# Kernel optimization log

Hardware: AMD Instinct MI355X
Metric: run time of the kernel (lower is better)

Reference implementation:

```python
import jax, jax.numpy as jnp
import numpy as np


def setup_inputs() -> dict:
    key = jax.random.key(0)
    k1, k2, k3, k4 = jax.random.split(key, 4)
    B, S, E, H = 8, 2048, 1024, 64
    x = jax.random.normal(k1, (B, S, E), dtype=jnp.float32)
    # nn.Linear(E, H, bias=False) weight is (H, E); we store transposed (E, H)
    scale = 1.0 / np.sqrt(E)
    Wk = jax.random.normal(k2, (E, H), dtype=jnp.float32) * scale
    Wq = jax.random.normal(k3, (E, H), dtype=jnp.float32) * scale
    Wv = jax.random.normal(k4, (E, H), dtype=jnp.float32) * scale
    return {"x": x, "Wk": Wk, "Wq": Wq, "Wv": Wv}


def reference(x, Wk, Wq, Wv):
    # x: (B, S, E); projections: (B, S, H)
    k = x @ Wk
    q = x @ Wq
    v = x @ Wv
    H = k.shape[-1]
    # scores: (B, S, S) with 1/sqrt(H) scaling as in the torch code
    scores = jnp.einsum("bqh,bkh->bqk", q, k) * (H ** -0.5)
    S = x.shape[1]
    causal = jnp.triu(jnp.full((S, S), -jnp.inf, dtype=scores.dtype), k=1)
    wei = jax.nn.softmax(scores + causal, axis=-1)
    # dropout p=0.0 -> identity
    return jnp.einsum("bqk,bkh->bqh", wei, v)
```

## Files before the change

kernel.cpp:

```cpp
#include <hip/hip_runtime.h>
#include <hip/hip_bf16.h>

typedef unsigned short ushort_t;
typedef __attribute__((ext_vector_type(8))) short short8;
typedef __attribute__((ext_vector_type(4))) short short4v;
typedef __attribute__((ext_vector_type(4))) float f32x4;

__device__ __forceinline__ float bf2f(ushort_t u) {
    unsigned int x = ((unsigned int)u) << 16;
    float f; __builtin_memcpy(&f, &x, 4); return f;
}
__device__ __forceinline__ ushort_t f2bf(float f) {
    __hip_bfloat16 h = __float2bfloat16(f);
    ushort_t u; __builtin_memcpy(&u, &h, 2); return u;
}
__device__ __forceinline__ unsigned packbf2(float a, float b) {
    return (unsigned)f2bf(a) | ((unsigned)f2bf(b) << 16);
}

__device__ __forceinline__ void gload16(const void* g, void* l) {
    __builtin_amdgcn_global_load_lds(
        (const __attribute__((address_space(1))) unsigned int*)g,
        (__attribute__((address_space(3))) unsigned int*)l, 16, 0, 0);
}

constexpr int E  = 1024;
constexpr int Hd = 64;
constexpr int S  = 2048;
constexpr int ROWS = 8 * 2048;
constexpr int NTOT = 192;
constexpr int LSTA = 88;
constexpr int BM   = 64;

__global__ __launch_bounds__(256)
void prep_wt(const float* __restrict__ Wk, const float* __restrict__ Wq,
             const float* __restrict__ Wv, ushort_t* __restrict__ WT)
{
    int idx = blockIdx.x * 256 + threadIdx.x;
    int n = idx >> 10;
    int kk = idx & 1023;
    const float* W = (n < 64) ? Wq : ((n < 128) ? Wk : Wv);
    int h = n & 63;
    WT[idx] = f2bf(W[kk * Hd + h]);
}

__global__ __launch_bounds__(512, 4)
void proj_v13(const float* __restrict__ x, const ushort_t* __restrict__ WT,
              ushort_t* __restrict__ qo, ushort_t* __restrict__ ko,
              ushort_t* __restrict__ vTo)
{
    __shared__ alignas(16) float    XS[2][BM * 64];
    __shared__ alignas(16) ushort_t WS[2][192 * 64];

    const int t    = threadIdx.x;
    const int w    = t >> 6;
    const int lane = t & 63;
    const int m    = lane & 15;
    const int g    = lane >> 4;
    const int rl   = m & 7;
    const int cg   = w & 3;
    const int mh   = w >> 2;
    const int rb   = blockIdx.x * BM;

    f32x4 accq[2], acck[2], accv[2];
    #pragma unroll
    for (int j = 0; j < 2; ++j) {
        accq[j] = (f32x4){0.f, 0.f, 0.f, 0.f};
        acck[j] = (f32x4){0.f, 0.f, 0.f, 0.f};
        accv[j] = (f32x4){0.f, 0.f, 0.f, 0.f};
    }

    const int xr0 = t >> 4,         xu0 = (t & 15) ^ (xr0 & 7);
    const int xr1 = (t + 512) >> 4, xu1 = (t & 15) ^ (xr1 & 7);
    const float* xsrc0 = x + (size_t)(rb + xr0) * E + xu0 * 4;
    const float* xsrc1 = x + (size_t)(rb + xr1) * E + xu1 * 4;

    const ushort_t* wsrc[3];
    #pragma unroll
    for (int j = 0; j < 3; ++j) {
        const int L  = j * 512 + t;
        const int wr = L >> 3;
        const int wu = (L & 7) ^ (wr & 7);
        wsrc[j] = WT + (size_t)wr * E + wu * 8;
    }

    int xiA[2][2], xiB[2][2];
    #pragma unroll
    for (int h = 0; h < 2; ++h)
        #pragma unroll
        for (int kt = 0; kt < 2; ++kt) {
            const int row = mh * 32 + h * 16 + m;
            const int U   = kt * 8 + 2 * g;
            xiA[h][kt] = (row * 16 + (U ^ rl)) * 4;
            xiB[h][kt] = (row * 16 + ((U + 1) ^ rl)) * 4;
        }
    int wiq[2], wik[2], wiv[2];
    #pragma unroll
    for (int kt = 0; kt < 2; ++kt) {
        const int U = kt * 4 + g;
        wiq[kt] = ((      cg * 16 + m) * 8 + (U ^ rl)) * 8;
        wik[kt] = ((64  + cg * 16 + m) * 8 + (U ^ rl)) * 8;
        wiv[kt] = ((128 + cg * 16 + m) * 8 + (U ^ rl)) * 8;
    }

    auto STAGE = [&](int buf, int c) {
        const int k0 = c * 64;
        char* xb = (char*)&XS[buf][0];
        char* wb = (char*)&WS[buf][0];
        gload16(xsrc0 + k0, xb + (size_t)t * 16);
        gload16(xsrc1 + k0, xb + (size_t)(t + 512) * 16);
        #pragma unroll
        for (int j = 0; j < 3; ++j)
            gload16(wsrc[j] + k0, wb + (size_t)(j * 512 + t) * 16);
    };

    auto COMPUTE = [&](int buf) {
        #pragma unroll
        for (int kt = 0; kt < 2; ++kt) {
            short8 fq = *(const short8*)&WS[buf][wiq[kt]];
            short8 fk = *(const short8*)&WS[buf][wik[kt]];
            short8 fv = *(const short8*)&WS[buf][wiv[kt]];
            #pragma unroll
            for (int h = 0; h < 2; ++h) {
                float4 A = *(const float4*)&XS[buf][xiA[h][kt]];
                float4 B = *(const float4*)&XS[buf][xiB[h][kt]];
                short8 a;
                {
                    unsigned u4[4];
                    u4[0] = packbf2(A.x, A.y);
                    u4[1] = packbf2(A.z, A.w);
                    u4[2] = packbf2(B.x, B.y);
                    u4[3] = packbf2(B.z, B.w);
                    __builtin_memcpy(&a, u4, 16);
                }
                accq[h] = __builtin_amdgcn_mfma_f32_16x16x32_bf16(a, fq, accq[h], 0, 0, 0);
                acck[h] = __builtin_amdgcn_mfma_f32_16x16x32_bf16(a, fk, acck[h], 0, 0, 0);
                accv[h] = __builtin_amdgcn_mfma_f32_16x16x32_bf16(fv, a, accv[h], 0, 0, 0);
            }
        }
    };

    STAGE(0, 0);
    STAGE(1, 1);

    #pragma unroll
    for (int i = 0; i < 16; ++i) {
        if (i < 15) { asm volatile("s_waitcnt vmcnt(5)" ::: "memory"); }
        else        { asm volatile("s_waitcnt vmcnt(0)" ::: "memory"); }
        __builtin_amdgcn_sched_barrier(0);
        __builtin_amdgcn_s_barrier();
        COMPUTE(i & 1);
        __builtin_amdgcn_s_barrier();
        if (i + 2 < 16) STAGE(i & 1, i + 2);
    }

    const int col   = cg * 16 + m;
    const int batch = rb >> 11;
    const int seq0  = rb & (S - 1);
    #pragma unroll
    for (int h = 0; h < 2; ++h) {
        const int orow = rb + mh * 32 + h * 16 + g * 4;
        #pragma unroll
        for (int r = 0; r < 4; ++r) {
            qo[(size_t)(orow + r) * Hd + col] = f2bf(accq[h][r] * 0.125f);
            ko[(size_t)(orow + r) * Hd + col] = f2bf(acck[h][r]);
        }
    }
    #pragma unroll
    for (int ns = 0; ns < 2; ++ns)
        #pragma unroll
        for (int r = 0; r < 4; ++r) {
            const int hc = cg * 16 + g * 4 + r;
            vTo[(size_t)batch * Hd * S + (size_t)hc * S + seq0 + mh * 32 + ns * 16 + m]
                = f2bf(accv[ns][r]);
        }
}

__global__ __launch_bounds__(256)
void attn_part(const ushort_t* __restrict__ q, const ushort_t* __restrict__ k,
               const ushort_t* __restrict__ vT,
               float* __restrict__ lp, ushort_t* __restrict__ op)
{
    const int bi     = blockIdx.x;
    const int parity = bi & 3;
    const int pr     = bi >> 2;
    const int batch  = pr & 7;
    const int tile   = 31 - (pr >> 3);
    const int qs0    = tile * 64;
    const int sidx   = (batch * 32 + tile) * 4 + parity;

    const ushort_t* kb  = k  + (size_t)batch * S * Hd;
    const ushort_t* vTb = vT + (size_t)batch * Hd * S;

    const int t    = threadIdx.x;
    const int w    = t >> 6;
    const int lane = t & 63;
    const int m    = lane & 15;
    const int g    = lane >> 4;

    __shared__ alignas(16) ushort_t KS [64][LSTA];
    __shared__ alignas(16) ushort_t VTS[64][LSTA];

    const ushort_t* qrow = q + (size_t)(batch * S + qs0 + w * 16 + m) * Hd;
    short8 qf0 = *(const short8*)(qrow + g * 8);
    short8 qf1 = *(const short8*)(qrow + 32 + g * 8);

    f32x4 o[4];
    #pragma unroll
    for (int j = 0; j < 4; ++j) o[j] = (f32x4){0.f, 0.f, 0.f, 0.f};
    float lrun = 0.f;
    const int qr = w * 16 + m;

    const int r1 = t >> 3, c16 = (t & 7) * 8;
    uint4 pk0, pk1, pv0, pv1;

    int c = parity;
    if (c <= tile) {
        const int key0 = c * 64;
        const ushort_t* kt_base = kb + (size_t)key0 * Hd;
        pk0 = *(const uint4*)(kt_base + t * 8);
        pk1 = *(const uint4*)(kt_base + (t + 256) * 8);
        pv0 = *(const uint4*)(vTb + (size_t)r1 * S + key0 + c16);
        pv1 = *(const uint4*)(vTb + (size_t)(r1 + 32) * S + key0 + c16);
    }

    for (; c <= tile; c += 4) {
        *(uint4*)&KS [r1][c16]       = pk0;
        *(uint4*)&KS [r1 + 32][c16]  = pk1;
        *(uint4*)&VTS[r1][c16]       = pv0;
        *(uint4*)&VTS[r1 + 32][c16]  = pv1;
        __syncthreads();

        if (c + 4 <= tile) {
            const int key0n = (c + 4) * 64;
            const ushort_t* kt_base = kb + (size_t)key0n * Hd;
            pk0 = *(const uint4*)(kt_base + t * 8);
            pk1 = *(const uint4*)(kt_base + (t + 256) * 8);
            pv0 = *(const uint4*)(vTb + (size_t)r1 * S + key0n + c16);
            pv1 = *(const uint4*)(vTb + (size_t)(r1 + 32) * S + key0n + c16);
        }

        f32x4 sacc[4];
        #pragma unroll
        for (int j = 0; j < 4; ++j) sacc[j] = (f32x4){0.f, 0.f, 0.f, 0.f};
        #pragma unroll
        for (int nt = 0; nt < 4; ++nt) {
            short8 b0 = *(const short8*)&KS[nt * 16 + m][g * 8];
            short8 b1 = *(const short8*)&KS[nt * 16 + m][32 + g * 8];
            sacc[nt] = __builtin_amdgcn_mfma_f32_16x16x32_bf16(b0, qf0, sacc[nt], 0, 0, 0);
            sacc[nt] = __builtin_amdgcn_mfma_f32_16x16x32_bf16(b1, qf1, sacc[nt], 0, 0, 0);
        }

        if (c == tile) {
            #pragma unroll
            for (int nt = 0; nt < 4; ++nt)
                #pragma unroll
                for (int r = 0; r < 4; ++r) {
                    const int keyl = nt * 16 + g * 4 + r;
                    sacc[nt][r] = (keyl > qr) ? 0.f : __expf(sacc[nt][r]);
                }
        } else {
            #pragma unroll
            for (int nt = 0; nt < 4; ++nt)
                #pragma unroll
                for (int r = 0; r < 4; ++r)
                    sacc[nt][r] = __expf(sacc[nt][r]);
        }

        #pragma unroll
        for (int nt = 0; nt < 4; ++nt)
            lrun += (sacc[nt][0] + sacc[nt][1]) + (sacc[nt][2] + sacc[nt][3]);

        unsigned pw0[4], pw1[4];
        #pragma unroll
        for (int s = 0; s < 4; ++s) {
            pw0[s] = packbf2(sacc[s][0], sacc[s][1]);
            pw1[s] = packbf2(sacc[s][2], sacc[s][3]);
        }

        #pragma unroll
        for (int s = 0; s < 4; ++s) {
            short4v pa;
            { unsigned u2[2] = {pw0[s], pw1[s]}; __builtin_memcpy(&pa, u2, 8); }
            #pragma unroll
            for (int nt = 0; nt < 4; ++nt) {
                short4v vb = *(const short4v*)&VTS[nt * 16 + m][s * 16 + g * 4];
                o[nt] = __builtin_amdgcn_mfma_f32_16x16x16bf16_1k(pa, vb, o[nt], 0, 0, 0);
            }
        }
        __syncthreads();
    }

    {
        float ts = lrun;
        ts += __shfl_xor(ts, 16, 64);
        ts += __shfl_xor(ts, 32, 64);
        if (lane < 16) lp[sidx * 64 + w * 16 + m] = ts;
    }
    #pragma unroll
    for (int nt = 0; nt < 4; ++nt)
        #pragma unroll
        for (int r = 0; r < 4; ++r)
            op[(size_t)sidx * 4096 + (w * 16 + g * 4 + r) * 64 + nt * 16 + m]
                = f2bf(o[nt][r]);
}

__global__ __launch_bounds__(256)
void attn_merge(const float* __restrict__ lp, const ushort_t* __restrict__ op,
                float* __restrict__ out)
{
    const int bq    = blockIdx.x;
    const int batch = bq >> 5;
    const int tile  = bq & 31;
    const int s0    = (batch * 32 + tile) * 4;

    const int t   = threadIdx.x;
    const int row = t >> 2;
    const int c16 = (t & 3) * 16;

    float l = 0.f;
    #pragma unroll
    for (int p = 0; p < 4; ++p) l += lp[(s0 + p) * 64 + row];
    const float inv = 1.f / l;

    float acc[16];
    #pragma unroll
    for (int j = 0; j < 16; ++j) acc[j] = 0.f;
    #pragma unroll
    for (int p = 0; p < 4; ++p) {
        short8 a0 = *(const short8*)(op + (size_t)(s0 + p) * 4096 + row * 64 + c16);
        short8 a1 = *(const short8*)(op + (size_t)(s0 + p) * 4096 + row * 64 + c16 + 8);
        #pragma unroll
        for (int j = 0; j < 8; ++j) {
            acc[j]     += bf2f((ushort_t)a0[j]);
            acc[j + 8] += bf2f((ushort_t)a1[j]);
        }
    }
    float* dst = out + (size_t)(batch * S + tile * 64 + row) * Hd + c16;
    #pragma unroll
    for (int j = 0; j < 16; ++j) dst[j] = acc[j] * inv;
}

extern "C" void kernel_launch(void* const* d_in, const int* in_sizes, int n_in,
                              void* d_out, int out_size, void* d_ws, size_t ws_size,
                              hipStream_t stream) {
    const float* x  = (const float*)d_in[0];
    const float* Wk = (const float*)d_in[1];
    const float* Wq = (const float*)d_in[2];
    const float* Wv = (const float*)d_in[3];
    float* out = (float*)d_out;

    ushort_t* qws  = (ushort_t*)d_ws;
    ushort_t* kws  = qws + (size_t)ROWS * Hd;
    ushort_t* vTws = kws + (size_t)ROWS * Hd;
    ushort_t* WT   = vTws + (size_t)ROWS * Hd;
    float*    lpp  = (float*)(WT + (size_t)NTOT * E);
    ushort_t* opp  = (ushort_t*)(lpp + 1024 * 64);

    prep_wt<<<(NTOT * E) / 256, 256, 0, stream>>>(Wk, Wq, Wv, WT);
    proj_v13<<<ROWS / BM, 512, 0, stream>>>(x, WT, qws, kws, vTws);
    attn_part<<<1024, 256, 0, stream>>>(qws, kws, vTws, lpp, opp);
    attn_merge<<<256, 256, 0, stream>>>(lpp, opp, out);
}
```

Measured before the change: 128.5 us.

## Load projection weights directly into registers and halve projection row tile

The projection kernel no longer stages the bf16 weight tile through LDS. Each wave now loads its q/k/v weight fragments straight from global memory into double-buffered registers, and only x goes through LDS. The row tile shrinks to 32 with 256-thread blocks, which doubles the grid and cuts LDS use. The aim is less LDS traffic and footprint and higher occupancy, at the cost of more global/L2 weight reads, since each block re-fetches the whole weight set for fewer rows.

Result: slower. 137.1 us (+6.6%).

```diff
diff --git a/kernel.cpp b/kernel.cpp
--- a/kernel.cpp
+++ b/kernel.cpp
@@ -30,7 +30,7 @@
 constexpr int ROWS = 8 * 2048;
 constexpr int NTOT = 192;
 constexpr int LSTA = 88;
-constexpr int BM   = 64;
+constexpr int BM   = 32;
 
 __global__ __launch_bounds__(256)
 void prep_wt(const float* __restrict__ Wk, const float* __restrict__ Wq,
@@ -44,13 +44,12 @@
     WT[idx] = f2bf(W[kk * Hd + h]);
 }
 
-__global__ __launch_bounds__(512, 4)
-void proj_v13(const float* __restrict__ x, const ushort_t* __restrict__ WT,
+__global__ __launch_bounds__(256, 2)
+void proj_v14(const float* __restrict__ x, const ushort_t* __restrict__ WT,
               ushort_t* __restrict__ qo, ushort_t* __restrict__ ko,
               ushort_t* __restrict__ vTo)
 {
-    __shared__ alignas(16) float    XS[2][BM * 64];
-    __shared__ alignas(16) ushort_t WS[2][192 * 64];
+    __shared__ alignas(16) float XS[2][BM * 64];
 
     const int t    = threadIdx.x;
     const int w    = t >> 6;
@@ -58,8 +57,6 @@
     const int m    = lane & 15;
     const int g    = lane >> 4;
     const int rl   = m & 7;
-    const int cg   = w & 3;
-    const int mh   = w >> 2;
     const int rb   = blockIdx.x * BM;
 
     f32x4 accq[2], acck[2], accv[2];
@@ -70,56 +67,47 @@
         accv[j] = (f32x4){0.f, 0.f, 0.f, 0.f};
     }
 
-    const int xr0 = t >> 4,         xu0 = (t & 15) ^ (xr0 & 7);
-    const int xr1 = (t + 512) >> 4, xu1 = (t & 15) ^ (xr1 & 7);
-    const float* xsrc0 = x + (size_t)(rb + xr0) * E + xu0 * 4;
-    const float* xsrc1 = x + (size_t)(rb + xr1) * E + xu1 * 4;
-
-    const ushort_t* wsrc[3];
-    #pragma unroll
-    for (int j = 0; j < 3; ++j) {
-        const int L  = j * 512 + t;
-        const int wr = L >> 3;
-        const int wu = (L & 7) ^ (wr & 7);
-        wsrc[j] = WT + (size_t)wr * E + wu * 8;
-    }
+    const int r0 = t >> 4,         u0 = (t & 15) ^ (r0 & 7);
+    const int r1 = (t + 256) >> 4, u1 = (t & 15) ^ (r1 & 7);
+    const float* xsrc0 = x + (size_t)(rb + r0) * E + u0 * 4;
+    const float* xsrc1 = x + (size_t)(rb + r1) * E + u1 * 4;
+
+    const ushort_t* wqp = WT + (size_t)(w * 16 + m) * E + g * 8;
+    const ushort_t* wkp = wqp + (size_t)64 * E;
+    const ushort_t* wvp = wqp + (size_t)128 * E;
 
     int xiA[2][2], xiB[2][2];
     #pragma unroll
     for (int h = 0; h < 2; ++h)
         #pragma unroll
         for (int kt = 0; kt < 2; ++kt) {
-            const int row = mh * 32 + h * 16 + m;
+            const int row = h * 16 + m;
             const int U   = kt * 8 + 2 * g;
             xiA[h][kt] = (row * 16 + (U ^ rl)) * 4;
             xiB[h][kt] = (row * 16 + ((U + 1) ^ rl)) * 4;
         }
-    int wiq[2], wik[2], wiv[2];
-    #pragma unroll
-    for (int kt = 0; kt < 2; ++kt) {
-        const int U = kt * 4 + g;
-        wiq[kt] = ((      cg * 16 + m) * 8 + (U ^ rl)) * 8;
-        wik[kt] = ((64  + cg * 16 + m) * 8 + (U ^ rl)) * 8;
-        wiv[kt] = ((128 + cg * 16 + m) * 8 + (U ^ rl)) * 8;
-    }
 
     auto STAGE = [&](int buf, int c) {
         const int k0 = c * 64;
         char* xb = (char*)&XS[buf][0];
-        char* wb = (char*)&WS[buf][0];
         gload16(xsrc0 + k0, xb + (size_t)t * 16);
-        gload16(xsrc1 + k0, xb + (size_t)(t + 512) * 16);
-        #pragma unroll
-        for (int j = 0; j < 3; ++j)
-            gload16(wsrc[j] + k0, wb + (size_t)(j * 512 + t) * 16);
+        gload16(xsrc1 + k0, xb + (size_t)(t + 256) * 16);
     };
 
-    auto COMPUTE = [&](int buf) {
+    auto WLOAD = [&](short8* wq, short8* wk, short8* wv, int c) {
+        const int k0 = c * 64;
         #pragma unroll
         for (int kt = 0; kt < 2; ++kt) {
-            short8 fq = *(const short8*)&WS[buf][wiq[kt]];
-            short8 fk = *(const short8*)&WS[buf][wik[kt]];
-            short8 fv = *(const short8*)&WS[buf][wiv[kt]];
+            wq[kt] = *(const short8*)(wqp + k0 + kt * 32);
+            wk[kt] = *(const short8*)(wkp + k0 + kt * 32);
+            wv[kt] = *(const short8*)(wvp + k0 + kt * 32);
+        }
+    };
+
+    auto COMPUTE = [&](int buf, const short8* wq, const short8* wk,
+                       const short8* wv) {
+        #pragma unroll
+        for (int kt = 0; kt < 2; ++kt) {
             #pragma unroll
             for (int h = 0; h < 2; ++h) {
                 float4 A = *(const float4*)&XS[buf][xiA[h][kt]];
@@ -133,33 +121,41 @@
                     u4[3] = packbf2(B.z, B.w);
                     __builtin_memcpy(&a, u4, 16);
                 }
-                accq[h] = __builtin_amdgcn_mfma_f32_16x16x32_bf16(a, fq, accq[h], 0, 0, 0);
-                acck[h] = __builtin_amdgcn_mfma_f32_16x16x32_bf16(a, fk, acck[h], 0, 0, 0);
-                accv[h] = __builtin_amdgcn_mfma_f32_16x16x32_bf16(fv, a, accv[h], 0, 0, 0);
+                accq[h] = __builtin_amdgcn_mfma_f32_16x16x32_bf16(a, wq[kt], accq[h], 0, 0, 0);
+                acck[h] = __builtin_amdgcn_mfma_f32_16x16x32_bf16(a, wk[kt], acck[h], 0, 0, 0);
+                accv[h] = __builtin_amdgcn_mfma_f32_16x16x32_bf16(wv[kt], a, accv[h], 0, 0, 0);
             }
         }
     };
 
-    STAGE(0, 0);
-    STAGE(1, 1);
+    short8 wqA[2], wkA[2], wvA[2], wqB[2], wkB[2], wvB[2];
+
+    STAGE(0, 0); WLOAD(wqA, wkA, wvA, 0);
+    STAGE(1, 1); WLOAD(wqB, wkB, wvB, 1);
 
     #pragma unroll
     for (int i = 0; i < 16; ++i) {
-        if (i < 15) { asm volatile("s_waitcnt vmcnt(5)" ::: "memory"); }
+        if (i < 15) { asm volatile("s_waitcnt vmcnt(8)" ::: "memory"); }
         else        { asm volatile("s_waitcnt vmcnt(0)" ::: "memory"); }
         __builtin_amdgcn_sched_barrier(0);
         __builtin_amdgcn_s_barrier();
-        COMPUTE(i & 1);
+        if ((i & 1) == 0) COMPUTE(0, wqA, wkA, wvA);
+        else              COMPUTE(1, wqB, wkB, wvB);
         __builtin_amdgcn_s_barrier();
-        if (i + 2 < 16) STAGE(i & 1, i + 2);
-    }
-
-    const int col   = cg * 16 + m;
+        if (i + 2 < 16) {
+            STAGE(i & 1, i + 2);
+            if ((i & 1) == 0) WLOAD(wqA, wkA, wvA, i + 2);
+            else              WLOAD(wqB, wkB, wvB, i + 2);
+            __builtin_amdgcn_sched_barrier(0);
+        }
+    }
+
+    const int col   = w * 16 + m;
     const int batch = rb >> 11;
     const int seq0  = rb & (S - 1);
     #pragma unroll
     for (int h = 0; h < 2; ++h) {
-        const int orow = rb + mh * 32 + h * 16 + g * 4;
+        const int orow = rb + h * 16 + g * 4;
         #pragma unroll
         for (int r = 0; r < 4; ++r) {
             qo[(size_t)(orow + r) * Hd + col] = f2bf(accq[h][r] * 0.125f);
@@ -170,8 +166,8 @@
     for (int ns = 0; ns < 2; ++ns)
         #pragma unroll
         for (int r = 0; r < 4; ++r) {
-            const int hc = cg * 16 + g * 4 + r;
-            vTo[(size_t)batch * Hd * S + (size_t)hc * S + seq0 + mh * 32 + ns * 16 + m]
+            const int hc = w * 16 + g * 4 + r;
+            vTo[(size_t)batch * Hd * S + (size_t)hc * S + seq0 + ns * 16 + m]
                 = f2bf(accv[ns][r]);
         }
 }
@@ -358,7 +354,7 @@
     ushort_t* opp  = (ushort_t*)(lpp + 1024 * 64);
 
     prep_wt<<<(NTOT * E) / 256, 256, 0, stream>>>(Wk, Wq, Wv, WT);
-    proj_v13<<<ROWS / BM, 512, 0, stream>>>(x, WT, qws, kws, vTws);
+    proj_v14<<<ROWS / BM, 256, 0, stream>>>(x, WT, qws, kws, vTws);
     attn_part<<<1024, 256, 0, stream>>>(qws, kws, vTws, lpp, opp);
     attn_merge<<<256, 256, 0, stream>>>(lpp, opp, out);
 }
```
